# Kernel optimization log

Hardware: AMD Instinct MI355X
Metric: run time of the kernel (lower is better)

The kernel has to match this reference:

```python
import jax, jax.numpy as jnp
import numpy as np

N_NODES = 100000
N_EDGES = 1600000
N_GRAPHS = 256
IN_C = 64
HID = 64


def _gcn_conv(x, W, b, src, dst, w, n):
    # GCNConv: x' = D^{-1/2} (A + I) D^{-1/2} (x W) + b, with edge weights w
    x = x @ W
    deg = jnp.zeros((n,), x.dtype).at[dst].add(w) + 1.0  # +1 for self-loop weight
    dinv = jax.lax.rsqrt(deg)
    norm = dinv[src] * w * dinv[dst]                      # [E]
    agg = jnp.zeros_like(x).at[dst].add(x[src] * norm[:, None])
    agg = agg + x * (1.0 / deg)[:, None]                  # self-loop term: d^{-1/2}*1*d^{-1/2}
    return agg + b


def setup_inputs() -> dict:
    key = jax.random.key(0)
    ks = jax.random.split(key, 16)
    inp = {
        "x": jax.random.normal(ks[0], (N_NODES, IN_C), jnp.float32),
        "edge_index": jax.random.randint(ks[1], (2, N_EDGES), 0, N_NODES, jnp.int32),
        "edge_weight": jax.random.uniform(ks[2], (N_EDGES,), jnp.float32),
        "batch": jnp.sort(jax.random.randint(ks[3], (N_NODES,), 0, N_GRAPHS, jnp.int32)),
    }
    s = 0.05
    inp["W0"] = jax.random.normal(ks[4], (IN_C, HID), jnp.float32) * s
    inp["b0"] = jnp.zeros((HID,), jnp.float32)
    inp["W1"] = jax.random.normal(ks[5], (HID, HID), jnp.float32) * s
    inp["b1"] = jnp.zeros((HID,), jnp.float32)
    inp["W2"] = jax.random.normal(ks[6], (HID, HID), jnp.float32) * s
    inp["b2"] = jnp.zeros((HID,), jnp.float32)
    inp["Wr0"] = jax.random.normal(ks[7], (HID, HID // 2), jnp.float32) * s
    inp["br0"] = jnp.zeros((HID // 2,), jnp.float32)
    inp["Wr1"] = jax.random.normal(ks[8], (HID // 2, 1), jnp.float32) * s
    inp["br1"] = jnp.zeros((1,), jnp.float32)
    return inp


def reference(x, edge_index, edge_weight, batch, W0, b0, W1, b1, W2, b2, Wr0, br0, Wr1, br1):
    n = x.shape[0]
    src, dst = edge_index[0], edge_index[1]
    h = jax.nn.relu(_gcn_conv(x, W0, b0, src, dst, edge_weight, n))
    h = jax.nn.relu(_gcn_conv(h, W1, b1, src, dst, edge_weight, n))
    h = _gcn_conv(h, W2, b2, src, dst, edge_weight, n)  # no activation on last GNN layer
    # MLP readout: hidden -> hidden//2 -> 1
    h = jax.nn.relu(h @ Wr0 + br0) @ Wr1 + br1          # [N, 1]
    # scatter-mean pooling by graph id
    sums = jax.ops.segment_sum(h, batch, num_segments=N_GRAPHS)
    cnt = jax.ops.segment_sum(jnp.ones((n, 1), h.dtype), batch, num_segments=N_GRAPHS)
    return sums / jnp.maximum(cnt, 1.0)
```

## Files before the change

kernel.cpp:

```cpp
#include <hip/hip_runtime.h>


#define NBK 391

__device__ __forceinline__ float bcastf(float v, int l) {
    return __int_as_float(__builtin_amdgcn_readlane(__float_as_int(v), l));
}

__global__ void hist_kernel(const int* __restrict__ dst,
                            int* __restrict__ bcnt, int ne) {
    __shared__ int h[512];
    for (int i = threadIdx.x; i < 512; i += blockDim.x) h[i] = 0;
    __syncthreads();
    int stride = gridDim.x * blockDim.x;
    for (int e = blockIdx.x * blockDim.x + threadIdx.x; e < ne; e += stride)
        atomicAdd(&h[dst[e] >> 8], 1);
    __syncthreads();
    for (int i = threadIdx.x; i < 512; i += blockDim.x)
        if (h[i]) atomicAdd(&bcnt[i], h[i]);
}

__global__ void bscan_kernel(const int* __restrict__ bcnt,
                             int* __restrict__ bbase,
                             int* __restrict__ gcur, int nb, int ne) {
    __shared__ int sh[512];
    int t = threadIdx.x;
    int v = (t < nb) ? bcnt[t] : 0;
    sh[t] = v;
    __syncthreads();
    for (int off = 1; off < 512; off <<= 1) {
        int u = (t >= off) ? sh[t - off] : 0;
        __syncthreads();
        sh[t] += u;
        __syncthreads();
    }
    if (t < nb) {
        int e = sh[t] - v;
        bbase[t] = e;
        gcur[t] = e;
    }
    if (t == 0) bbase[nb] = ne;
}

__global__ void scatterB_kernel(const int* __restrict__ src,
                                const int* __restrict__ dst,
                                const float* __restrict__ ew,
                                int* __restrict__ gcur,
                                int2* __restrict__ packed, int ne) {
    __shared__ int h[512];
    __shared__ int cur[512];
    int chunk = (ne + gridDim.x - 1) / gridDim.x;
    int e0 = blockIdx.x * chunk;
    int e1 = e0 + chunk; if (e1 > ne) e1 = ne;
    for (int i = threadIdx.x; i < 512; i += blockDim.x) h[i] = 0;
    __syncthreads();
    for (int e = e0 + threadIdx.x; e < e1; e += blockDim.x)
        atomicAdd(&h[dst[e] >> 8], 1);
    __syncthreads();
    for (int i = threadIdx.x; i < 512; i += blockDim.x)
        cur[i] = h[i] ? atomicAdd(&gcur[i], h[i]) : 0;
    __syncthreads();
    for (int e = e0 + threadIdx.x; e < e1; e += blockDim.x) {
        int d = dst[e];
        int pos = atomicAdd(&cur[d >> 8], 1);
        int2 v;
        v.x = ((d & 255) << 24) | src[e];
        v.y = __float_as_int(ew[e]);
        packed[pos] = v;
    }
}

__global__ void bucket_build_kernel(const int2* __restrict__ packed,
                                    const int* __restrict__ bbase,
                                    int* __restrict__ rptr,
                                    int* __restrict__ cnt,
                                    float* __restrict__ dinv,
                                    int2* __restrict__ csr, int n) {
    __shared__ int cl[256];
    __shared__ int sc[256];
    __shared__ int cur[256];
    int b = blockIdx.x;
    int t = threadIdx.x;
    int node0 = b << 8;
    int nn = n - node0; if (nn > 256) nn = 256;
    int ebase = bbase[b];
    int m = bbase[b + 1] - ebase;
    cl[t] = 0;
    __syncthreads();
    for (int j = t; j < m; j += 256) {
        int local = ((unsigned)packed[ebase + j].x) >> 24;
        atomicAdd(&cl[local], 1);
    }
    __syncthreads();
    int c = cl[t];
    sc[t] = c;
    __syncthreads();
    for (int off = 1; off < 256; off <<= 1) {
        int u = (t >= off) ? sc[t - off] : 0;
        __syncthreads();
        sc[t] += u;
        __syncthreads();
    }
    int base = ebase + sc[t] - c;
    cur[t] = base;
    if (t < nn) {
        rptr[node0 + t] = base;
        cnt[node0 + t] = c;
    }
    __syncthreads();
    for (int j = t; j < m; j += 256) {
        int2 p = packed[ebase + j];
        int local = ((unsigned)p.x) >> 24;
        int pos = atomicAdd(&cur[local], 1);
        int2 v;
        v.x = p.x & 0x00FFFFFF;
        v.y = p.y;
        csr[pos] = v;
    }
    __syncthreads();
    if (t < nn) {
        float s = 0.0f;
        for (int j = base; j < base + c; ++j)
            s += __int_as_float(csr[j].y);
        dinv[node0 + t] = 1.0f / sqrtf(s + 1.0f);
    }
}

template <bool RELU>
__global__ void __launch_bounds__(256, 4)
gemm_rl_kernel(const float* __restrict__ X, const float* W,
               const float* __restrict__ dinv, float* __restrict__ Ts,
               int n) {
    __shared__ float Wl[4096];
    {
        const float4* Wv = (const float4*)W;
        float4* Lv = (float4*)Wl;
        for (int i = threadIdx.x; i < 1024; i += 256) Lv[i] = Wv[i];
    }
    __syncthreads();
    int lane = threadIdx.x & 63;
    int wid  = (blockIdx.x * blockDim.x + threadIdx.x) >> 6;
    int nw   = (gridDim.x * blockDim.x) >> 6;
    int lrow = lane >> 4;
    int lcol = (lane & 15) * 4;
    for (int r0 = wid * 4; r0 + 4 <= n; r0 += nw * 4) {
        float4 xv = *(const float4*)&X[(size_t)(r0 + lrow) * 64 + lcol];
        if (RELU) {
            xv.x = fmaxf(xv.x, 0.f); xv.y = fmaxf(xv.y, 0.f);
            xv.z = fmaxf(xv.z, 0.f); xv.w = fmaxf(xv.w, 0.f);
        }
        float a0 = 0.f, a1 = 0.f, a2 = 0.f, a3 = 0.f;
#pragma unroll
        for (int k4 = 0; k4 < 16; ++k4) {
            float w0 = Wl[(4 * k4 + 0) * 64 + lane];
            float w1 = Wl[(4 * k4 + 1) * 64 + lane];
            float w2 = Wl[(4 * k4 + 2) * 64 + lane];
            float w3 = Wl[(4 * k4 + 3) * 64 + lane];
            a0 = fmaf(bcastf(xv.x, k4), w0, a0);
            a0 = fmaf(bcastf(xv.y, k4), w1, a0);
            a0 = fmaf(bcastf(xv.z, k4), w2, a0);
            a0 = fmaf(bcastf(xv.w, k4), w3, a0);
            a1 = fmaf(bcastf(xv.x, 16 + k4), w0, a1);
            a1 = fmaf(bcastf(xv.y, 16 + k4), w1, a1);
            a1 = fmaf(bcastf(xv.z, 16 + k4), w2, a1);
            a1 = fmaf(bcastf(xv.w, 16 + k4), w3, a1);
            a2 = fmaf(bcastf(xv.x, 32 + k4), w0, a2);
            a2 = fmaf(bcastf(xv.y, 32 + k4), w1, a2);
            a2 = fmaf(bcastf(xv.z, 32 + k4), w2, a2);
            a2 = fmaf(bcastf(xv.w, 32 + k4), w3, a2);
            a3 = fmaf(bcastf(xv.x, 48 + k4), w0, a3);
            a3 = fmaf(bcastf(xv.y, 48 + k4), w1, a3);
            a3 = fmaf(bcastf(xv.z, 48 + k4), w2, a3);
            a3 = fmaf(bcastf(xv.w, 48 + k4), w3, a3);
        }
        Ts[(size_t)(r0 + 0) * 64 + lane] = a0 * dinv[r0 + 0];
        Ts[(size_t)(r0 + 1) * 64 + lane] = a1 * dinv[r0 + 1];
        Ts[(size_t)(r0 + 2) * 64 + lane] = a2 * dinv[r0 + 2];
        Ts[(size_t)(r0 + 3) * 64 + lane] = a3 * dinv[r0 + 3];
    }
    if (wid == 0) {
        for (int r = (n & ~3); r < n; ++r) {
            const float4* xr = (const float4*)(X + (size_t)r * 64);
            float acc = 0.f;
#pragma unroll
            for (int k4 = 0; k4 < 16; ++k4) {
                float4 a = xr[k4];
                if (RELU) {
                    a.x = fmaxf(a.x, 0.f); a.y = fmaxf(a.y, 0.f);
                    a.z = fmaxf(a.z, 0.f); a.w = fmaxf(a.w, 0.f);
                }
                acc = fmaf(a.x, Wl[(4 * k4 + 0) * 64 + lane], acc);
                acc = fmaf(a.y, Wl[(4 * k4 + 1) * 64 + lane], acc);
                acc = fmaf(a.z, Wl[(4 * k4 + 2) * 64 + lane], acc);
                acc = fmaf(a.w, Wl[(4 * k4 + 3) * 64 + lane], acc);
            }
            Ts[(size_t)r * 64 + lane] = acc * dinv[r];
        }
    }
}

__global__ void __launch_bounds__(256, 4)
fgather_kernel(const int2* __restrict__ csr,
               const int* __restrict__ rptr,
               const int* __restrict__ cnt,
               const float* __restrict__ dinv,
               const float* __restrict__ b,
               const float* __restrict__ Ts_in,
               const float* Wn,
               float* __restrict__ Ts_out, int n) {
    __shared__ float Wl[4096];
    {
        const float4* Wv = (const float4*)Wn;
        float4* Lv = (float4*)Wl;
        for (int i = threadIdx.x; i < 1024; i += 256) Lv[i] = Wv[i];
    }
    __syncthreads();
    int lane = threadIdx.x & 63;
    int r = (int)(((size_t)blockIdx.x * blockDim.x + threadIdx.x) >> 6);
    if (r >= n) return;
    int sub = lane >> 4;
    int cl  = lane & 15;
    int start = rptr[r];
    int m = cnt[r];
    float4 a0 = {0.f, 0.f, 0.f, 0.f};
    float4 a1 = {0.f, 0.f, 0.f, 0.f};
    float4 a2 = {0.f, 0.f, 0.f, 0.f};
    float4 a3 = {0.f, 0.f, 0.f, 0.f};
    int j = sub;
    for (; j + 12 < m; j += 16) {
        int2 e0 = csr[start + j];
        int2 e1 = csr[start + j + 4];
        int2 e2 = csr[start + j + 8];
        int2 e3 = csr[start + j + 12];
        float w0 = __int_as_float(e0.y);
        float w1 = __int_as_float(e1.y);
        float w2 = __int_as_float(e2.y);
        float w3 = __int_as_float(e3.y);
        float4 t0 = *(const float4*)&Ts_in[(size_t)e0.x * 64 + cl * 4];
        float4 t1 = *(const float4*)&Ts_in[(size_t)e1.x * 64 + cl * 4];
        float4 t2 = *(const float4*)&Ts_in[(size_t)e2.x * 64 + cl * 4];
        float4 t3 = *(const float4*)&Ts_in[(size_t)e3.x * 64 + cl * 4];
        a0.x = fmaf(t0.x, w0, a0.x); a0.y = fmaf(t0.y, w0, a0.y);
        a0.z = fmaf(t0.z, w0, a0.z); a0.w = fmaf(t0.w, w0, a0.w);
        a1.x = fmaf(t1.x, w1, a1.x); a1.y = fmaf(t1.y, w1, a1.y);
        a1.z = fmaf(t1.z, w1, a1.z); a1.w = fmaf(t1.w, w1, a1.w);
        a2.x = fmaf(t2.x, w2, a2.x); a2.y = fmaf(t2.y, w2, a2.y);
        a2.z = fmaf(t2.z, w2, a2.z); a2.w = fmaf(t2.w, w2, a2.w);
        a3.x = fmaf(t3.x, w3, a3.x); a3.y = fmaf(t3.y, w3, a3.y);
        a3.z = fmaf(t3.z, w3, a3.z); a3.w = fmaf(t3.w, w3, a3.w);
    }
    for (; j < m; j += 4) {
        int2 e0 = csr[start + j];
        float w0 = __int_as_float(e0.y);
        float4 t0 = *(const float4*)&Ts_in[(size_t)e0.x * 64 + cl * 4];
        a0.x = fmaf(t0.x, w0, a0.x); a0.y = fmaf(t0.y, w0, a0.y);
        a0.z = fmaf(t0.z, w0, a0.z); a0.w = fmaf(t0.w, w0, a0.w);
    }
    a0.x += a1.x + a2.x + a3.x;
    a0.y += a1.y + a2.y + a3.y;
    a0.z += a1.z + a2.z + a3.z;
    a0.w += a1.w + a2.w + a3.w;
#pragma unroll
    for (int off = 16; off < 64; off <<= 1) {
        a0.x += __shfl_xor(a0.x, off);
        a0.y += __shfl_xor(a0.y, off);
        a0.z += __shfl_xor(a0.z, off);
        a0.w += __shfl_xor(a0.w, off);
    }
    float dv = dinv[r];
    float4 ts = *(const float4*)&Ts_in[(size_t)r * 64 + cl * 4];
    float4 bb = *(const float4*)&b[cl * 4];
    float tx = fmaxf(fmaf(dv, a0.x + ts.x, bb.x), 0.f);
    float ty = fmaxf(fmaf(dv, a0.y + ts.y, bb.y), 0.f);
    float tz = fmaxf(fmaf(dv, a0.z + ts.z, bb.z), 0.f);
    float tw = fmaxf(fmaf(dv, a0.w + ts.w, bb.w), 0.f);
    float c0 = 0.f, c1 = 0.f, c2 = 0.f, c3 = 0.f;
#pragma unroll
    for (int q = 0; q < 16; ++q) {
        c0 = fmaf(bcastf(tx, q), Wl[(4 * q + 0) * 64 + lane], c0);
        c1 = fmaf(bcastf(ty, q), Wl[(4 * q + 1) * 64 + lane], c1);
        c2 = fmaf(bcastf(tz, q), Wl[(4 * q + 2) * 64 + lane], c2);
        c3 = fmaf(bcastf(tw, q), Wl[(4 * q + 3) * 64 + lane], c3);
    }
    Ts_out[(size_t)r * 64 + lane] = ((c0 + c1) + (c2 + c3)) * dv;
}

__global__ void __launch_bounds__(256, 4)
rgather_kernel(const int2* __restrict__ csr,
               const int* __restrict__ rptr,
               const int* __restrict__ cnt,
               const float* __restrict__ dinv,
               const float* __restrict__ b,
               const float* __restrict__ Ts,
               const float* Wr0, const float* br0,
               const float* Wr1, const float* br1,
               float* __restrict__ svbuf, int n) {
    __shared__ float Wl[64 * 32];
    __shared__ float w1s[32];
    __shared__ float b0s[32];
    {
        const float4* Wv = (const float4*)Wr0;
        float4* Lv = (float4*)Wl;
        for (int i = threadIdx.x; i < 512; i += 256) Lv[i] = Wv[i];
        if (threadIdx.x < 32) {
            w1s[threadIdx.x] = Wr1[threadIdx.x];
            b0s[threadIdx.x] = br0[threadIdx.x];
        }
    }
    __syncthreads();
    int lane = threadIdx.x & 63;
    int r = (int)(((size_t)blockIdx.x * blockDim.x + threadIdx.x) >> 6);
    if (r >= n) return;
    int sub = lane >> 4;
    int cl  = lane & 15;
    int start = rptr[r];
    int m = cnt[r];
    float4 a0 = {0.f, 0.f, 0.f, 0.f};
    float4 a1 = {0.f, 0.f, 0.f, 0.f};
    float4 a2 = {0.f, 0.f, 0.f, 0.f};
    float4 a3 = {0.f, 0.f, 0.f, 0.f};
    int j = sub;
    for (; j + 12 < m; j += 16) {
        int2 e0 = csr[start + j];
        int2 e1 = csr[start + j + 4];
        int2 e2 = csr[start + j + 8];
        int2 e3 = csr[start + j + 12];
        float w0 = __int_as_float(e0.y);
        float w1 = __int_as_float(e1.y);
        float w2 = __int_as_float(e2.y);
        float w3 = __int_as_float(e3.y);
        float4 t0 = *(const float4*)&Ts[(size_t)e0.x * 64 + cl * 4];
        float4 t1 = *(const float4*)&Ts[(size_t)e1.x * 64 + cl * 4];
        float4 t2 = *(const float4*)&Ts[(size_t)e2.x * 64 + cl * 4];
        float4 t3 = *(const float4*)&Ts[(size_t)e3.x * 64 + cl * 4];
        a0.x = fmaf(t0.x, w0, a0.x); a0.y = fmaf(t0.y, w0, a0.y);
        a0.z = fmaf(t0.z, w0, a0.z); a0.w = fmaf(t0.w, w0, a0.w);
        a1.x = fmaf(t1.x, w1, a1.x); a1.y = fmaf(t1.y, w1, a1.y);
        a1.z = fmaf(t1.z, w1, a1.z); a1.w = fmaf(t1.w, w1, a1.w);
        a2.x = fmaf(t2.x, w2, a2.x); a2.y = fmaf(t2.y, w2, a2.y);
        a2.z = fmaf(t2.z, w2, a2.z); a2.w = fmaf(t2.w, w2, a2.w);
        a3.x = fmaf(t3.x, w3, a3.x); a3.y = fmaf(t3.y, w3, a3.y);
        a3.z = fmaf(t3.z, w3, a3.z); a3.w = fmaf(t3.w, w3, a3.w);
    }
    for (; j < m; j += 4) {
        int2 e0 = csr[start + j];
        float w0 = __int_as_float(e0.y);
        float4 t0 = *(const float4*)&Ts[(size_t)e0.x * 64 + cl * 4];
        a0.x = fmaf(t0.x, w0, a0.x); a0.y = fmaf(t0.y, w0, a0.y);
        a0.z = fmaf(t0.z, w0, a0.z); a0.w = fmaf(t0.w, w0, a0.w);
    }
    a0.x += a1.x + a2.x + a3.x;
    a0.y += a1.y + a2.y + a3.y;
    a0.z += a1.z + a2.z + a3.z;
    a0.w += a1.w + a2.w + a3.w;
#pragma unroll
    for (int off = 16; off < 64; off <<= 1) {
        a0.x += __shfl_xor(a0.x, off);
        a0.y += __shfl_xor(a0.y, off);
        a0.z += __shfl_xor(a0.z, off);
        a0.w += __shfl_xor(a0.w, off);
    }
    float dv = dinv[r];
    float4 ts = *(const float4*)&Ts[(size_t)r * 64 + cl * 4];
    float4 bb = *(const float4*)&b[cl * 4];
    float tx = fmaf(dv, a0.x + ts.x, bb.x);
    float ty = fmaf(dv, a0.y + ts.y, bb.y);
    float tz = fmaf(dv, a0.z + ts.z, bb.z);
    float tw = fmaf(dv, a0.w + ts.w, bb.w);
    int hj = lane & 31;
    float c0 = 0.f, c1 = 0.f, c2 = 0.f, c3 = 0.f;
#pragma unroll
    for (int q = 0; q < 16; ++q) {
        c0 = fmaf(bcastf(tx, q), Wl[(4 * q + 0) * 32 + hj], c0);
        c1 = fmaf(bcastf(ty, q), Wl[(4 * q + 1) * 32 + hj], c1);
        c2 = fmaf(bcastf(tz, q), Wl[(4 * q + 2) * 32 + hj], c2);
        c3 = fmaf(bcastf(tw, q), Wl[(4 * q + 3) * 32 + hj], c3);
    }
    float h = fmaxf(((c0 + c1) + (c2 + c3)) + b0s[hj], 0.f);
    float p = h * w1s[hj];
#pragma unroll
    for (int off = 1; off < 32; off <<= 1) p += __shfl_xor(p, off);
    if (lane == 0) svbuf[r] = p + br1[0];
}

__global__ void segpool_kernel(const float* __restrict__ svbuf,
                               const int* __restrict__ batch,
                               float* __restrict__ gsum,
                               float* __restrict__ gcnt, int n) {
    int r = blockIdx.x * blockDim.x + threadIdx.x;
    int lane = threadIdx.x & 63;
    float sv = 0.0f;
    int g = -1;
    if (r < n) { sv = svbuf[r]; g = batch[r]; }
    float c = (r < n) ? 1.0f : 0.0f;
#pragma unroll
    for (int off = 1; off < 64; off <<= 1) {
        int   og = __shfl_down(g, off);
        float ov = __shfl_down(sv, off);
        float oc = __shfl_down(c, off);
        if ((lane + off) < 64 && og == g) { sv += ov; c += oc; }
    }
    int gprev = __shfl_up(g, 1);
    bool head = (lane == 0) || (gprev != g);
    if (head && g >= 0) {
        atomicAdd(&gsum[g], sv);
        atomicAdd(&gcnt[g], c);
    }
}

__global__ void pool_fin_kernel(const float* __restrict__ gsum,
                                const float* __restrict__ gcnt,
                                float* __restrict__ out, int ng) {
    int g = blockIdx.x * blockDim.x + threadIdx.x;
    if (g < ng) out[g] = gsum[g] / fmaxf(gcnt[g], 1.0f);
}

extern "C" void kernel_launch(void* const* d_in, const int* in_sizes, int n_in,
                              void* d_out, int out_size, void* d_ws, size_t ws_size,
                              hipStream_t stream) {
    const float* x    = (const float*)d_in[0];
    const int*   ei   = (const int*)d_in[1];
    const float* ew   = (const float*)d_in[2];
    const int*   batch= (const int*)d_in[3];
    const float* W0   = (const float*)d_in[4];
    const float* b0   = (const float*)d_in[5];
    const float* W1   = (const float*)d_in[6];
    const float* b1   = (const float*)d_in[7];
    const float* W2   = (const float*)d_in[8];
    const float* b2   = (const float*)d_in[9];
    const float* Wr0  = (const float*)d_in[10];
    const float* br0  = (const float*)d_in[11];
    const float* Wr1  = (const float*)d_in[12];
    const float* br1  = (const float*)d_in[13];
    float* out = (float*)d_out;

    int n  = in_sizes[0] / 64;
    int ne = in_sizes[1] / 2;
    int ng = out_size;
    const int* srcv = ei;
    const int* dstv = ei + ne;
    int nbk = (n + 255) >> 8;

    char* ws = (char*)d_ws;
    size_t off = 0;
    auto alloc = [&](size_t bytes) {
        void* p = ws + off;
        off += (bytes + 255) & ~(size_t)255;
        return p;
    };
    float* Ts     = (float*)alloc((size_t)n * 64 * sizeof(float));
    float* A      = (float*)alloc((size_t)n * 64 * sizeof(float));
    float* dinv   = (float*)alloc((size_t)n * sizeof(float));
    float* svbuf  = (float*)alloc((size_t)n * sizeof(float));
    int*   cnt    = (int*)alloc((size_t)n * sizeof(int));
    int*   rptr   = (int*)alloc((size_t)n * sizeof(int));
    int*   bcnt   = (int*)alloc(520 * sizeof(int));
    int*   bbase  = (int*)alloc(520 * sizeof(int));
    int*   gcur   = (int*)alloc(520 * sizeof(int));
    int2*  csr    = (int2*)alloc((size_t)ne * sizeof(int2));
    float* gsum   = (float*)alloc((size_t)ng * sizeof(float));
    float* gcnt   = (float*)alloc((size_t)ng * sizeof(float));
    int2*  packed = (int2*)Ts;
    (void)ws_size;

    hipMemsetAsync(bcnt, 0, 520 * sizeof(int), stream);
    hipMemsetAsync(gsum, 0, (size_t)ng * sizeof(float), stream);
    hipMemsetAsync(gcnt, 0, (size_t)ng * sizeof(float), stream);

    hist_kernel<<<256, 256, 0, stream>>>(dstv, bcnt, ne);
    bscan_kernel<<<1, 512, 0, stream>>>(bcnt, bbase, gcur, nbk, ne);
    scatterB_kernel<<<200, 256, 0, stream>>>(srcv, dstv, ew, gcur, packed, ne);
    bucket_build_kernel<<<nbk, 256, 0, stream>>>(packed, bbase, rptr, cnt,
                                                 dinv, csr, n);

    const int gemm_blocks = 2048;
    unsigned gat_blocks = (unsigned)(((size_t)n * 64 + 255) / 256);

    gemm_rl_kernel<false><<<gemm_blocks, 256, 0, stream>>>(x, W0, dinv, Ts, n);
    fgather_kernel<<<gat_blocks, 256, 0, stream>>>(csr, rptr, cnt, dinv, b0,
                                                   Ts, W1, A, n);
    fgather_kernel<<<gat_blocks, 256, 0, stream>>>(csr, rptr, cnt, dinv, b1,
                                                   A, W2, Ts, n);
    rgather_kernel<<<gat_blocks, 256, 0, stream>>>(csr, rptr, cnt, dinv, b2,
                                                   Ts, Wr0, br0, Wr1, br1,
                                                   svbuf, n);
    segpool_kernel<<<(n + 255) / 256, 256, 0, stream>>>(svbuf, batch,
                                                        gsum, gcnt, n);
    pool_fin_kernel<<<(ng + 255) / 256, 256, 0, stream>>>(gsum, gcnt, out, ng);
}
```

Measured before the change: 355.9 us.

## Fuse pooling into readout gather, share node features via LDS, retune grids

```diff
diff --git a/kernel.cpp b/kernel.cpp
--- a/kernel.cpp
+++ b/kernel.cpp
@@ -209,6 +209,7 @@
                const float* Wn,
                float* __restrict__ Ts_out, int n) {
     __shared__ float Wl[4096];
+    __shared__ float tbuf[4][64];
     {
         const float4* Wv = (const float4*)Wn;
         float4* Lv = (float4*)Wl;
@@ -216,6 +217,7 @@
     }
     __syncthreads();
     int lane = threadIdx.x & 63;
+    int w = threadIdx.x >> 6;
     int r = (int)(((size_t)blockIdx.x * blockDim.x + threadIdx.x) >> 6);
     if (r >= n) return;
     int sub = lane >> 4;
@@ -270,17 +272,22 @@
     float dv = dinv[r];
     float4 ts = *(const float4*)&Ts_in[(size_t)r * 64 + cl * 4];
     float4 bb = *(const float4*)&b[cl * 4];
-    float tx = fmaxf(fmaf(dv, a0.x + ts.x, bb.x), 0.f);
-    float ty = fmaxf(fmaf(dv, a0.y + ts.y, bb.y), 0.f);
-    float tz = fmaxf(fmaf(dv, a0.z + ts.z, bb.z), 0.f);
-    float tw = fmaxf(fmaf(dv, a0.w + ts.w, bb.w), 0.f);
+    if (sub == 0) {
+        float4 tq;
+        tq.x = fmaxf(fmaf(dv, a0.x + ts.x, bb.x), 0.f);
+        tq.y = fmaxf(fmaf(dv, a0.y + ts.y, bb.y), 0.f);
+        tq.z = fmaxf(fmaf(dv, a0.z + ts.z, bb.z), 0.f);
+        tq.w = fmaxf(fmaf(dv, a0.w + ts.w, bb.w), 0.f);
+        *(float4*)&tbuf[w][cl * 4] = tq;
+    }
     float c0 = 0.f, c1 = 0.f, c2 = 0.f, c3 = 0.f;
 #pragma unroll
     for (int q = 0; q < 16; ++q) {
-        c0 = fmaf(bcastf(tx, q), Wl[(4 * q + 0) * 64 + lane], c0);
-        c1 = fmaf(bcastf(ty, q), Wl[(4 * q + 1) * 64 + lane], c1);
-        c2 = fmaf(bcastf(tz, q), Wl[(4 * q + 2) * 64 + lane], c2);
-        c3 = fmaf(bcastf(tw, q), Wl[(4 * q + 3) * 64 + lane], c3);
+        float4 tq = *(const float4*)&tbuf[w][q * 4];
+        c0 = fmaf(tq.x, Wl[(4 * q + 0) * 64 + lane], c0);
+        c1 = fmaf(tq.y, Wl[(4 * q + 1) * 64 + lane], c1);
+        c2 = fmaf(tq.z, Wl[(4 * q + 2) * 64 + lane], c2);
+        c3 = fmaf(tq.w, Wl[(4 * q + 3) * 64 + lane], c3);
     }
     Ts_out[(size_t)r * 64 + lane] = ((c0 + c1) + (c2 + c3)) * dv;
 }
@@ -294,10 +301,13 @@
                const float* __restrict__ Ts,
                const float* Wr0, const float* br0,
                const float* Wr1, const float* br1,
-               float* __restrict__ svbuf, int n) {
+               const int* __restrict__ batch,
+               float* __restrict__ gsum,
+               float* __restrict__ gcnt, int n) {
     __shared__ float Wl[64 * 32];
     __shared__ float w1s[32];
     __shared__ float b0s[32];
+    __shared__ float tbuf[4][64];
     {
         const float4* Wv = (const float4*)Wr0;
         float4* Lv = (float4*)Wl;
@@ -309,6 +319,7 @@
     }
     __syncthreads();
     int lane = threadIdx.x & 63;
+    int w = threadIdx.x >> 6;
     int r = (int)(((size_t)blockIdx.x * blockDim.x + threadIdx.x) >> 6);
     if (r >= n) return;
     int sub = lane >> 4;
@@ -363,48 +374,32 @@
     float dv = dinv[r];
     float4 ts = *(const float4*)&Ts[(size_t)r * 64 + cl * 4];
     float4 bb = *(const float4*)&b[cl * 4];
-    float tx = fmaf(dv, a0.x + ts.x, bb.x);
-    float ty = fmaf(dv, a0.y + ts.y, bb.y);
-    float tz = fmaf(dv, a0.z + ts.z, bb.z);
-    float tw = fmaf(dv, a0.w + ts.w, bb.w);
+    if (sub == 0) {
+        float4 tq;
+        tq.x = fmaf(dv, a0.x + ts.x, bb.x);
+        tq.y = fmaf(dv, a0.y + ts.y, bb.y);
+        tq.z = fmaf(dv, a0.z + ts.z, bb.z);
+        tq.w = fmaf(dv, a0.w + ts.w, bb.w);
+        *(float4*)&tbuf[w][cl * 4] = tq;
+    }
     int hj = lane & 31;
     float c0 = 0.f, c1 = 0.f, c2 = 0.f, c3 = 0.f;
 #pragma unroll
     for (int q = 0; q < 16; ++q) {
-        c0 = fmaf(bcastf(tx, q), Wl[(4 * q + 0) * 32 + hj], c0);
-        c1 = fmaf(bcastf(ty, q), Wl[(4 * q + 1) * 32 + hj], c1);
-        c2 = fmaf(bcastf(tz, q), Wl[(4 * q + 2) * 32 + hj], c2);
-        c3 = fmaf(bcastf(tw, q), Wl[(4 * q + 3) * 32 + hj], c3);
+        float4 tq = *(const float4*)&tbuf[w][q * 4];
+        c0 = fmaf(tq.x, Wl[(4 * q + 0) * 32 + hj], c0);
+        c1 = fmaf(tq.y, Wl[(4 * q + 1) * 32 + hj], c1);
+        c2 = fmaf(tq.z, Wl[(4 * q + 2) * 32 + hj], c2);
+        c3 = fmaf(tq.w, Wl[(4 * q + 3) * 32 + hj], c3);
     }
     float h = fmaxf(((c0 + c1) + (c2 + c3)) + b0s[hj], 0.f);
     float p = h * w1s[hj];
 #pragma unroll
     for (int off = 1; off < 32; off <<= 1) p += __shfl_xor(p, off);
-    if (lane == 0) svbuf[r] = p + br1[0];
-}
-
-__global__ void segpool_kernel(const float* __restrict__ svbuf,
-                               const int* __restrict__ batch,
-                               float* __restrict__ gsum,
-                               float* __restrict__ gcnt, int n) {
-    int r = blockIdx.x * blockDim.x + threadIdx.x;
-    int lane = threadIdx.x & 63;
-    float sv = 0.0f;
-    int g = -1;
-    if (r < n) { sv = svbuf[r]; g = batch[r]; }
-    float c = (r < n) ? 1.0f : 0.0f;
-#pragma unroll
-    for (int off = 1; off < 64; off <<= 1) {
-        int   og = __shfl_down(g, off);
-        float ov = __shfl_down(sv, off);
-        float oc = __shfl_down(c, off);
-        if ((lane + off) < 64 && og == g) { sv += ov; c += oc; }
-    }
-    int gprev = __shfl_up(g, 1);
-    bool head = (lane == 0) || (gprev != g);
-    if (head && g >= 0) {
-        atomicAdd(&gsum[g], sv);
-        atomicAdd(&gcnt[g], c);
+    if (lane == 0) {
+        int g = batch[r];
+        atomicAdd(&gsum[g], p + br1[0]);
+        atomicAdd(&gcnt[g], 1.0f);
     }
 }
 
@@ -451,7 +446,6 @@
     float* Ts     = (float*)alloc((size_t)n * 64 * sizeof(float));
     float* A      = (float*)alloc((size_t)n * 64 * sizeof(float));
     float* dinv   = (float*)alloc((size_t)n * sizeof(float));
-    float* svbuf  = (float*)alloc((size_t)n * sizeof(float));
     int*   cnt    = (int*)alloc((size_t)n * sizeof(int));
     int*   rptr   = (int*)alloc((size_t)n * sizeof(int));
     int*   bcnt   = (int*)alloc(520 * sizeof(int));
@@ -467,9 +461,9 @@
     hipMemsetAsync(gsum, 0, (size_t)ng * sizeof(float), stream);
     hipMemsetAsync(gcnt, 0, (size_t)ng * sizeof(float), stream);
 
-    hist_kernel<<<256, 256, 0, stream>>>(dstv, bcnt, ne);
+    hist_kernel<<<1024, 256, 0, stream>>>(dstv, bcnt, ne);
     bscan_kernel<<<1, 512, 0, stream>>>(bcnt, bbase, gcur, nbk, ne);
-    scatterB_kernel<<<200, 256, 0, stream>>>(srcv, dstv, ew, gcur, packed, ne);
+    scatterB_kernel<<<256, 256, 0, stream>>>(srcv, dstv, ew, gcur, packed, ne);
     bucket_build_kernel<<<nbk, 256, 0, stream>>>(packed, bbase, rptr, cnt,
                                                  dinv, csr, n);
 
@@ -483,8 +477,6 @@
                                                    A, W2, Ts, n);
     rgather_kernel<<<gat_blocks, 256, 0, stream>>>(csr, rptr, cnt, dinv, b2,
                                                    Ts, Wr0, br0, Wr1, br1,
-                                                   svbuf, n);
-    segpool_kernel<<<(n + 255) / 256, 256, 0, stream>>>(svbuf, batch,
-                                                        gsum, gcnt, n);
+                                                   batch, gsum, gcnt, n);
     pool_fin_kernel<<<(ng + 255) / 256, 256, 0, stream>>>(gsum, gcnt, out, ng);
 }
```

Result: slower. 749.5 us (+110.6%).
